# Optimization experiments

Hardware: AMD Instinct MI355X
Metric: run time of the kernel (lower is better)

The kernel has to match this reference:

```python
import jax, jax.numpy as jnp
import numpy as np

IN_FEATURES = 4096
OUT_FEATURES = 4096
BATCH, SEQ = 4, 2048

def setup_inputs() -> dict:
    key = jax.random.key(0)
    k1, k2, k3, k4, k5 = jax.random.split(key, 5)
    x = jax.random.normal(k1, (BATCH, SEQ, IN_FEATURES), dtype=jnp.float32)
    # int8 codes stored as int32 in [0, 255] (asymmetric uint8-style quantization)
    qweight = jax.random.randint(k2, (OUT_FEATURES, IN_FEATURES), 0, 255, dtype=jnp.int32)
    scales = jax.random.uniform(k3, (OUT_FEATURES,), dtype=jnp.float32) * 0.01 + 1e-3
    zero_points = jax.random.uniform(k4, (OUT_FEATURES,), dtype=jnp.float32) * 255.0
    bias = jax.random.normal(k5, (OUT_FEATURES,), dtype=jnp.float32)
    return {"x": x, "qweight": qweight, "scales": scales, "zero_points": zero_points, "bias": bias}

def reference(x, qweight, scales, zero_points, bias):
    # Per-output-channel dequantization: W[o, i] = (q[o, i] - zp[o]) * scale[o]
    w = (qweight.astype(jnp.float32) - zero_points[:, None]) * scales[:, None]  # [O, I]
    # y = x @ W.T + b, fused dequant + GEMM in the original ipex op
    y = jnp.einsum("bsi,oi->bso", x, w) + bias
    return y
```

## Files before the change

kernel.cpp:

```cpp
#include <hip/hip_runtime.h>
#include <hip/hip_bf16.h>

typedef __attribute__((ext_vector_type(4))) int i32x4;

#define M_DIM 8192
#define N_DIM 4096
#define K_DIM 4096
#define BM 256
#define BN 256
#define BK 128
#define NT2 (K_DIM / BK)

static __device__ inline void gload_lds16(const void* g, void* l) {
  __builtin_amdgcn_global_load_lds(
      (const __attribute__((address_space(1))) unsigned int*)g,
      (__attribute__((address_space(3))) unsigned int*)l,
      16, 0, 0);
}

__global__ __launch_bounds__(256) void prep_x_i8(
    const float* __restrict__ x, char* __restrict__ xq,
    float* __restrict__ rx, float* __restrict__ sxf) {
  const int row = blockIdx.x;
  const int tid = threadIdx.x;
  const float4* xr = (const float4*)(x + (long)row * K_DIM);
  float4 v[4];
  float mx = 0.f;
#pragma unroll
  for (int i = 0; i < 4; ++i) {
    v[i] = xr[i * 256 + tid];
    mx = fmaxf(mx, fmaxf(fmaxf(fabsf(v[i].x), fabsf(v[i].y)),
                         fmaxf(fabsf(v[i].z), fabsf(v[i].w))));
  }
#pragma unroll
  for (int off = 32; off > 0; off >>= 1) mx = fmaxf(mx, __shfl_down(mx, off, 64));
  __shared__ float redm[4];
  __shared__ int reds[4];
  const int lane = tid & 63, w = tid >> 6;
  if (lane == 0) redm[w] = mx;
  __syncthreads();
  const float maxv = fmaxf(fmaxf(redm[0], redm[1]), fmaxf(redm[2], redm[3]));
  const float inv = maxv > 0.f ? 127.f / maxv : 0.f;
  int* xo = (int*)(xq + (long)row * K_DIM);
  int ssum = 0;
#pragma unroll
  for (int i = 0; i < 4; ++i) {
    const int q0 = __float2int_rn(v[i].x * inv);
    const int q1 = __float2int_rn(v[i].y * inv);
    const int q2 = __float2int_rn(v[i].z * inv);
    const int q3 = __float2int_rn(v[i].w * inv);
    ssum += q0 + q1 + q2 + q3;
    xo[i * 256 + tid] =
        (q0 & 255) | ((q1 & 255) << 8) | ((q2 & 255) << 16) | ((q3 & 255) << 24);
  }
#pragma unroll
  for (int off = 32; off > 0; off >>= 1) ssum += __shfl_down(ssum, off, 64);
  if (lane == 0) reds[w] = ssum;
  __syncthreads();
  if (tid == 0) {
    rx[row] = maxv * (1.f / 127.f);
    sxf[row] = (float)(reds[0] + reds[1] + reds[2] + reds[3]);
  }
}

__global__ __launch_bounds__(256) void prep_q_i8(
    const int* __restrict__ q, char* __restrict__ qb) {
  const long idx = (long)blockIdx.x * blockDim.x + threadIdx.x;
  const int4 v = ((const int4*)q)[idx];
  const int a = v.x - 128, b = v.y - 128, c = v.z - 128, d = v.w - 128;
  ((int*)qb)[idx] = (a & 255) | ((b & 255) << 8) | ((c & 255) << 16) | ((d & 255) << 24);
}

__global__ __launch_bounds__(512, 2) void wq_gemm_i8(
    const char* __restrict__ A,
    const char* __restrict__ B,
    const float* __restrict__ rx,
    const float* __restrict__ sxf,
    const float* __restrict__ scales,
    const float* __restrict__ zps,
    const float* __restrict__ bias,
    float* __restrict__ C) {
  __shared__ __align__(16) char lds[2 * 65536];

  const int tid = threadIdx.x;
  const int lane = tid & 63;
  const int wv = tid >> 6;
  const int wr = wv >> 2, wc = wv & 3;

  const int wg = blockIdx.x;
  const int lid = (wg & 7) * 64 + (wg >> 3);
  const int bx = lid & 15, by = lid >> 4;
  const int brow = by * BM;
  const int bcol = bx * BN;

  i32x4 acc[8][4] = {};

  const int srow = tid >> 3;
  const int schunk = ((tid & 7) ^ (srow & 7)) * 16;
  const int wub = (tid & ~63) * 16;
  const char* gAs = A + (long)(brow + srow) * K_DIM + schunk;
  const char* gBs = B + (long)(bcol + srow) * K_DIM + schunk;

#define STAGE_A2(T, J0, J1)                                                   \
  do {                                                                        \
    char* d = lds + ((T) & 1) * 65536;                                        \
    gload_lds16(gAs + (long)(J0) * 262144 + (long)(T) * 128,                  \
                d + (J0) * 8192 + wub);                                       \
    gload_lds16(gAs + (long)(J1) * 262144 + (long)(T) * 128,                  \
                d + (J1) * 8192 + wub);                                       \
  } while (0)
#define STAGE_B2(T, J0, J1)                                                   \
  do {                                                                        \
    char* d = lds + ((T) & 1) * 65536 + 32768;                                \
    gload_lds16(gBs + (long)(J0) * 262144 + (long)(T) * 128,                  \
                d + (J0) * 8192 + wub);                                       \
    gload_lds16(gBs + (long)(J1) * 262144 + (long)(T) * 128,                  \
                d + (J1) * 8192 + wub);                                       \
  } while (0)

  const int row15 = lane & 15;
  const int kq = lane >> 4;
  int aoff[2], boff[2];
#pragma unroll
  for (int ks = 0; ks < 2; ++ks) {
    const int ch = ((ks * 4 + kq) ^ (row15 & 7)) * 16;
    aoff[ks] = (wr * 128 + row15) * 128 + ch;
    boff[ks] = 32768 + (wc * 64 + row15) * 128 + ch;
  }

#define RD_A(BB, FM, KS) (*(const i32x4*)(lds + (BB) + aoff[KS] + (FM) * 2048))
#define RD_B(BB, FN, KS) (*(const i32x4*)(lds + (BB) + boff[KS] + (FN) * 2048))
#define MMA(FM, FN, AV, BV)                                                   \
  acc[FM][FN] = __builtin_amdgcn_mfma_i32_16x16x64_i8(AV, BV, acc[FM][FN], 0, 0, 0)

#define BAR() __builtin_amdgcn_s_barrier()
#define VMC(N)                                                                \
  do {                                                                        \
    asm volatile("s_waitcnt vmcnt(" #N ")");                                  \
    __builtin_amdgcn_sched_barrier(0);                                        \
  } while (0)

#define HALF_MMA(BB, FM0, AF, BF)                                             \
  do {                                                                        \
    _Pragma("unroll") for (int f = 0; f < 4; ++f)                             \
      _Pragma("unroll") for (int ks = 0; ks < 2; ++ks)                        \
        AF[f][ks] = RD_A(BB, (FM0) + f, ks);                                  \
    _Pragma("unroll") for (int ks = 0; ks < 2; ++ks)                          \
      _Pragma("unroll") for (int f = 0; f < 4; ++f)                           \
        _Pragma("unroll") for (int n = 0; n < 4; ++n)                         \
          MMA((FM0) + f, n, AF[f][ks], BF[n][ks]);                            \
  } while (0)

  STAGE_A2(0, 0, 2);
  STAGE_B2(0, 0, 2);
  STAGE_B2(0, 1, 3);
  STAGE_A2(0, 1, 3);
  VMC(2);
  BAR();

  i32x4 af[4][2], bf[4][2];

  for (int t = 0; t < NT2 - 1; ++t) {
    const int bb = (t & 1) * 65536;
    const int t1 = t + 1;
#pragma unroll
    for (int n = 0; n < 4; ++n)
#pragma unroll
      for (int ks = 0; ks < 2; ++ks) bf[n][ks] = RD_B(bb, n, ks);
    STAGE_A2(t1, 0, 2);
    STAGE_B2(t1, 0, 2);
    STAGE_B2(t1, 1, 3);
    HALF_MMA(bb, 0, af, bf);
    VMC(6);
    BAR();
    STAGE_A2(t1, 1, 3);
    HALF_MMA(bb, 4, af, bf);
    VMC(2);
    BAR();
  }

  {
    const int bb = 65536;
#pragma unroll
    for (int n = 0; n < 4; ++n)
#pragma unroll
      for (int ks = 0; ks < 2; ++ks) bf[n][ks] = RD_B(bb, n, ks);
    HALF_MMA(bb, 0, af, bf);
    VMC(0);
    BAR();
    HALF_MMA(bb, 4, af, bf);
  }

  float sc[4], zp[4], bs[4];
  int coln[4];
#pragma unroll
  for (int fn = 0; fn < 4; ++fn) {
    coln[fn] = bcol + wc * 64 + fn * 16 + row15;
    sc[fn] = scales[coln[fn]];
    zp[fn] = 128.f - zps[coln[fn]];
    bs[fn] = bias[coln[fn]];
  }
#pragma unroll
  for (int fm = 0; fm < 8; ++fm) {
    const int r0 = brow + wr * 128 + fm * 16 + kq * 4;
#pragma unroll
    for (int j = 0; j < 4; ++j) {
      const int grow = r0 + j;
      const float rxv = rx[grow];
      const float sxv = sxf[grow];
#pragma unroll
      for (int fn = 0; fn < 4; ++fn) {
        C[(long)grow * N_DIM + coln[fn]] =
            sc[fn] * rxv * ((float)acc[fm][fn][j] + zp[fn] * sxv) + bs[fn];
      }
    }
  }
}

extern "C" void kernel_launch(void* const* d_in, const int* in_sizes, int n_in,
                              void* d_out, int out_size, void* d_ws, size_t ws_size,
                              hipStream_t stream) {
  const float* x = (const float*)d_in[0];
  const int* qw = (const int*)d_in[1];
  const float* scales = (const float*)d_in[2];
  const float* zps = (const float*)d_in[3];
  const float* bias = (const float*)d_in[4];
  float* out = (float*)d_out;

  char* ws = (char*)d_ws;
  char* xq = ws;
  char* qb = ws + (size_t)32 * 1024 * 1024;
  float* rx = (float*)(ws + (size_t)48 * 1024 * 1024);
  float* sxf = (float*)(ws + (size_t)48 * 1024 * 1024 + 65536);

  hipLaunchKernelGGL(prep_x_i8, dim3(M_DIM), dim3(256), 0, stream, x, xq, rx, sxf);
  hipLaunchKernelGGL(prep_q_i8, dim3((N_DIM * K_DIM / 4) / 256), dim3(256), 0, stream,
                     qw, qb);
  hipLaunchKernelGGL(wq_gemm_i8, dim3((M_DIM / BM) * (N_DIM / BN)), dim3(512), 0,
                     stream, xq, qb, rx, sxf, scales, zps, bias, out);
}
```

Before: 179.8 us.

## Use four waves with 128x128 warp tiles and a simplified double-buffer loop

The GEMM block drops from 8 waves to 4 waves, and each wave now computes a 128x128 sub-tile instead of 128x64. This doubles the accumulator count per wave and reduces the LDS fragment reads per MFMA. The split-phase staging schedule is replaced by a simpler one: each k-step issues the next tile's loads, waits for the current tile, then computes. The epilogue now loads scales, zero points and bias per element instead of hoisting them. In exchange, fewer waves per CU leave less room to hide latency, register pressure rises sharply, and load and compute overlap is coarser.

```diff
diff --git a/kernel.cpp b/kernel.cpp
--- a/kernel.cpp
+++ b/kernel.cpp
@@ -71,7 +71,7 @@
   ((int*)qb)[idx] = (a & 255) | ((b & 255) << 8) | ((c & 255) << 16) | ((d & 255) << 24);
 }
 
-__global__ __launch_bounds__(512, 2) void wq_gemm_i8(
+__global__ __launch_bounds__(256, 1) void wq_gemm_i8(
     const char* __restrict__ A,
     const char* __restrict__ B,
     const float* __restrict__ rx,
@@ -85,7 +85,7 @@
   const int tid = threadIdx.x;
   const int lane = tid & 63;
   const int wv = tid >> 6;
-  const int wr = wv >> 2, wc = wv & 3;
+  const int wr = wv >> 1, wc = wv & 1;
 
   const int wg = blockIdx.x;
   const int lid = (wg & 7) * 64 + (wg >> 3);
@@ -93,7 +93,7 @@
   const int brow = by * BM;
   const int bcol = bx * BN;
 
-  i32x4 acc[8][4] = {};
+  i32x4 acc[8][8] = {};
 
   const int srow = tid >> 3;
   const int schunk = ((tid & 7) ^ (srow & 7)) * 16;
@@ -101,21 +101,15 @@
   const char* gAs = A + (long)(brow + srow) * K_DIM + schunk;
   const char* gBs = B + (long)(bcol + srow) * K_DIM + schunk;
 
-#define STAGE_A2(T, J0, J1)                                                   \
+#define STAGE(T)                                                              \
   do {                                                                        \
     char* d = lds + ((T) & 1) * 65536;                                        \
-    gload_lds16(gAs + (long)(J0) * 262144 + (long)(T) * 128,                  \
-                d + (J0) * 8192 + wub);                                       \
-    gload_lds16(gAs + (long)(J1) * 262144 + (long)(T) * 128,                  \
-                d + (J1) * 8192 + wub);                                       \
-  } while (0)
-#define STAGE_B2(T, J0, J1)                                                   \
-  do {                                                                        \
-    char* d = lds + ((T) & 1) * 65536 + 32768;                                \
-    gload_lds16(gBs + (long)(J0) * 262144 + (long)(T) * 128,                  \
-                d + (J0) * 8192 + wub);                                       \
-    gload_lds16(gBs + (long)(J1) * 262144 + (long)(T) * 128,                  \
-                d + (J1) * 8192 + wub);                                       \
+    _Pragma("unroll") for (int j = 0; j < 8; ++j)                             \
+      gload_lds16(gAs + (long)j * 131072 + (long)(T) * 128,                   \
+                  d + j * 4096 + wub);                                        \
+    _Pragma("unroll") for (int j = 0; j < 8; ++j)                             \
+      gload_lds16(gBs + (long)j * 131072 + (long)(T) * 128,                   \
+                  d + 32768 + j * 4096 + wub);                                \
   } while (0)
 
   const int row15 = lane & 15;
@@ -125,7 +119,7 @@
   for (int ks = 0; ks < 2; ++ks) {
     const int ch = ((ks * 4 + kq) ^ (row15 & 7)) * 16;
     aoff[ks] = (wr * 128 + row15) * 128 + ch;
-    boff[ks] = 32768 + (wc * 64 + row15) * 128 + ch;
+    boff[ks] = 32768 + (wc * 128 + row15) * 128 + ch;
   }
 
 #define RD_A(BB, FM, KS) (*(const i32x4*)(lds + (BB) + aoff[KS] + (FM) * 2048))
@@ -140,66 +134,40 @@
     __builtin_amdgcn_sched_barrier(0);                                        \
   } while (0)
 
-#define HALF_MMA(BB, FM0, AF, BF)                                             \
+#define COMPUTE(BB)                                                           \
   do {                                                                        \
-    _Pragma("unroll") for (int f = 0; f < 4; ++f)                             \
+    i32x4 bf[8][2];                                                           \
+    _Pragma("unroll") for (int n = 0; n < 8; ++n)                             \
       _Pragma("unroll") for (int ks = 0; ks < 2; ++ks)                        \
-        AF[f][ks] = RD_A(BB, (FM0) + f, ks);                                  \
-    _Pragma("unroll") for (int ks = 0; ks < 2; ++ks)                          \
-      _Pragma("unroll") for (int f = 0; f < 4; ++f)                           \
-        _Pragma("unroll") for (int n = 0; n < 4; ++n)                         \
-          MMA((FM0) + f, n, AF[f][ks], BF[n][ks]);                            \
+        bf[n][ks] = RD_B(BB, n, ks);                                          \
+    _Pragma("unroll") for (int f = 0; f < 8; ++f) {                           \
+      i32x4 a0 = RD_A(BB, f, 0), a1 = RD_A(BB, f, 1);                         \
+      _Pragma("unroll") for (int n = 0; n < 8; ++n) {                         \
+        MMA(f, n, a0, bf[n][0]);                                              \
+        MMA(f, n, a1, bf[n][1]);                                              \
+      }                                                                       \
+    }                                                                         \
   } while (0)
 
-  STAGE_A2(0, 0, 2);
-  STAGE_B2(0, 0, 2);
-  STAGE_B2(0, 1, 3);
-  STAGE_A2(0, 1, 3);
-  VMC(2);
+  STAGE(0);
+  VMC(0);
   BAR();
-
-  i32x4 af[4][2], bf[4][2];
 
   for (int t = 0; t < NT2 - 1; ++t) {
     const int bb = (t & 1) * 65536;
-    const int t1 = t + 1;
-#pragma unroll
-    for (int n = 0; n < 4; ++n)
-#pragma unroll
-      for (int ks = 0; ks < 2; ++ks) bf[n][ks] = RD_B(bb, n, ks);
-    STAGE_A2(t1, 0, 2);
-    STAGE_B2(t1, 0, 2);
-    STAGE_B2(t1, 1, 3);
-    HALF_MMA(bb, 0, af, bf);
-    VMC(6);
+    STAGE(t + 1);
+    VMC(16);
     BAR();
-    STAGE_A2(t1, 1, 3);
-    HALF_MMA(bb, 4, af, bf);
-    VMC(2);
+    COMPUTE(bb);
     BAR();
   }
 
   {
-    const int bb = 65536;
-#pragma unroll
-    for (int n = 0; n < 4; ++n)
-#pragma unroll
-      for (int ks = 0; ks < 2; ++ks) bf[n][ks] = RD_B(bb, n, ks);
-    HALF_MMA(bb, 0, af, bf);
     VMC(0);
     BAR();
-    HALF_MMA(bb, 4, af, bf);
-  }
-
-  float sc[4], zp[4], bs[4];
-  int coln[4];
-#pragma unroll
-  for (int fn = 0; fn < 4; ++fn) {
-    coln[fn] = bcol + wc * 64 + fn * 16 + row15;
-    sc[fn] = scales[coln[fn]];
-    zp[fn] = 128.f - zps[coln[fn]];
-    bs[fn] = bias[coln[fn]];
-  }
+    COMPUTE(((NT2 - 1) & 1) * 65536);
+  }
+
 #pragma unroll
   for (int fm = 0; fm < 8; ++fm) {
     const int r0 = brow + wr * 128 + fm * 16 + kq * 4;
@@ -209,9 +177,11 @@
       const float rxv = rx[grow];
       const float sxv = sxf[grow];
 #pragma unroll
-      for (int fn = 0; fn < 4; ++fn) {
-        C[(long)grow * N_DIM + coln[fn]] =
-            sc[fn] * rxv * ((float)acc[fm][fn][j] + zp[fn] * sxv) + bs[fn];
+      for (int fn = 0; fn < 8; ++fn) {
+        const int coln = bcol + wc * 128 + fn * 16 + row15;
+        C[(long)grow * N_DIM + coln] =
+            scales[coln] * rxv * ((float)acc[fm][fn][j] + (128.f - zps[coln]) * sxv) +
+            bias[coln];
       }
     }
   }
@@ -236,6 +206,6 @@
   hipLaunchKernelGGL(prep_x_i8, dim3(M_DIM), dim3(256), 0, stream, x, xq, rx, sxf);
   hipLaunchKernelGGL(prep_q_i8, dim3((N_DIM * K_DIM / 4) / 256), dim3(256), 0, stream,
                      qw, qb);
-  hipLaunchKernelGGL(wq_gemm_i8, dim3((M_DIM / BM) * (N_DIM / BN)), dim3(512), 0,
+  hipLaunchKernelGGL(wq_gemm_i8, dim3((M_DIM / BM) * (N_DIM / BN)), dim3(256), 0,
                      stream, xq, qb, rx, sxf, scales, zps, bias, out);
 }
```

Measured after the change: 255.1 us. 1.42x slower.

## Load B operand directly into registers and halve LDS staging buffers

Applied to the files above, without the earlier changes.

The weight (B) tile is no longer staged through LDS. Each wave now reads its B fragments from global memory straight into registers, while only A is double-buffered in LDS. This halves LDS use, which may let two workgroups fit per CU, and cuts the loop to one barrier per K-step. The cost is that the two wave rows in a block load the same B data twice, and the B loads are issued just before they are consumed, so global-memory latency can land on the MFMA path.

```diff
diff --git a/kernel.cpp b/kernel.cpp
--- a/kernel.cpp
+++ b/kernel.cpp
@@ -80,7 +80,7 @@
     const float* __restrict__ zps,
     const float* __restrict__ bias,
     float* __restrict__ C) {
-  __shared__ __align__(16) char lds[2 * 65536];
+  __shared__ __align__(16) char lds[2 * 32768];
 
   const int tid = threadIdx.x;
   const int lane = tid & 63;
@@ -99,37 +99,26 @@
   const int schunk = ((tid & 7) ^ (srow & 7)) * 16;
   const int wub = (tid & ~63) * 16;
   const char* gAs = A + (long)(brow + srow) * K_DIM + schunk;
-  const char* gBs = B + (long)(bcol + srow) * K_DIM + schunk;
-
-#define STAGE_A2(T, J0, J1)                                                   \
-  do {                                                                        \
-    char* d = lds + ((T) & 1) * 65536;                                        \
-    gload_lds16(gAs + (long)(J0) * 262144 + (long)(T) * 128,                  \
-                d + (J0) * 8192 + wub);                                       \
-    gload_lds16(gAs + (long)(J1) * 262144 + (long)(T) * 128,                  \
-                d + (J1) * 8192 + wub);                                       \
-  } while (0)
-#define STAGE_B2(T, J0, J1)                                                   \
-  do {                                                                        \
-    char* d = lds + ((T) & 1) * 65536 + 32768;                                \
-    gload_lds16(gBs + (long)(J0) * 262144 + (long)(T) * 128,                  \
-                d + (J0) * 8192 + wub);                                       \
-    gload_lds16(gBs + (long)(J1) * 262144 + (long)(T) * 128,                  \
-                d + (J1) * 8192 + wub);                                       \
+
+#define STAGE_A4(T)                                                           \
+  do {                                                                        \
+    char* d = lds + ((T) & 1) * 32768;                                        \
+    gload_lds16(gAs + (long)(T) * 128, d + wub);                              \
+    gload_lds16(gAs + 262144 + (long)(T) * 128, d + 8192 + wub);              \
+    gload_lds16(gAs + 524288 + (long)(T) * 128, d + 16384 + wub);             \
+    gload_lds16(gAs + 786432 + (long)(T) * 128, d + 24576 + wub);             \
   } while (0)
 
   const int row15 = lane & 15;
   const int kq = lane >> 4;
-  int aoff[2], boff[2];
+  int aoff[2];
 #pragma unroll
   for (int ks = 0; ks < 2; ++ks) {
     const int ch = ((ks * 4 + kq) ^ (row15 & 7)) * 16;
     aoff[ks] = (wr * 128 + row15) * 128 + ch;
-    boff[ks] = 32768 + (wc * 64 + row15) * 128 + ch;
   }
 
 #define RD_A(BB, FM, KS) (*(const i32x4*)(lds + (BB) + aoff[KS] + (FM) * 2048))
-#define RD_B(BB, FN, KS) (*(const i32x4*)(lds + (BB) + boff[KS] + (FN) * 2048))
 #define MMA(FM, FN, AV, BV)                                                   \
   acc[FM][FN] = __builtin_amdgcn_mfma_i32_16x16x64_i8(AV, BV, acc[FM][FN], 0, 0, 0)
 
@@ -140,55 +129,50 @@
     __builtin_amdgcn_sched_barrier(0);                                        \
   } while (0)
 
-#define HALF_MMA(BB, FM0, AF, BF)                                             \
+  const char* Bp = B + (long)(bcol + wc * 64 + row15) * K_DIM + kq * 16;
+
+  i32x4 bf[4][2];
+
+#define LDB(T)                                                                \
+  do {                                                                        \
+    const char* bp = Bp + (long)(T) * 128;                                    \
+    _Pragma("unroll") for (int n = 0; n < 4; ++n)                             \
+      _Pragma("unroll") for (int ks = 0; ks < 2; ++ks)                        \
+        bf[n][ks] = *(const i32x4*)(bp + (long)n * 65536 + ks * 64);          \
+  } while (0)
+
+  i32x4 af[4][2];
+#define HALF_MMA(BB, FM0)                                                     \
   do {                                                                        \
     _Pragma("unroll") for (int f = 0; f < 4; ++f)                             \
       _Pragma("unroll") for (int ks = 0; ks < 2; ++ks)                        \
-        AF[f][ks] = RD_A(BB, (FM0) + f, ks);                                  \
+        af[f][ks] = RD_A(BB, (FM0) + f, ks);                                  \
     _Pragma("unroll") for (int ks = 0; ks < 2; ++ks)                          \
       _Pragma("unroll") for (int f = 0; f < 4; ++f)                           \
         _Pragma("unroll") for (int n = 0; n < 4; ++n)                         \
-          MMA((FM0) + f, n, AF[f][ks], BF[n][ks]);                            \
-  } while (0)
-
-  STAGE_A2(0, 0, 2);
-  STAGE_B2(0, 0, 2);
-  STAGE_B2(0, 1, 3);
-  STAGE_A2(0, 1, 3);
-  VMC(2);
+          MMA((FM0) + f, n, af[f][ks], bf[n][ks]);                            \
+  } while (0)
+
+  STAGE_A4(0);
+  LDB(0);
+  VMC(8);
   BAR();
 
-  i32x4 af[4][2], bf[4][2];
-
   for (int t = 0; t < NT2 - 1; ++t) {
-    const int bb = (t & 1) * 65536;
+    const int bb = (t & 1) * 32768;
     const int t1 = t + 1;
-#pragma unroll
-    for (int n = 0; n < 4; ++n)
-#pragma unroll
-      for (int ks = 0; ks < 2; ++ks) bf[n][ks] = RD_B(bb, n, ks);
-    STAGE_A2(t1, 0, 2);
-    STAGE_B2(t1, 0, 2);
-    STAGE_B2(t1, 1, 3);
-    HALF_MMA(bb, 0, af, bf);
-    VMC(6);
+    STAGE_A4(t1);
+    HALF_MMA(bb, 0);
+    HALF_MMA(bb, 4);
+    LDB(t1);
+    VMC(8);
     BAR();
-    STAGE_A2(t1, 1, 3);
-    HALF_MMA(bb, 4, af, bf);
-    VMC(2);
-    BAR();
   }
 
   {
-    const int bb = 65536;
-#pragma unroll
-    for (int n = 0; n < 4; ++n)
-#pragma unroll
-      for (int ks = 0; ks < 2; ++ks) bf[n][ks] = RD_B(bb, n, ks);
-    HALF_MMA(bb, 0, af, bf);
-    VMC(0);
-    BAR();
-    HALF_MMA(bb, 4, af, bf);
+    const int bb = ((NT2 - 1) & 1) * 32768;
+    HALF_MMA(bb, 0);
+    HALF_MMA(bb, 4);
   }
 
   float sc[4], zp[4], bs[4];
```

After: 247.4 us. 1.38x slower.
